# Performance work log

Hardware: AMD Instinct MI355X
Metric: run time of the kernel (lower is better)

Reference implementation:

```python
import jax, jax.numpy as jnp
import numpy as np

B_SZ, SEQ = 2, 4096
D_MODEL = 1024
EXPAND = 2
HEADDIM = 64
D_STATE = 128
D_CONV = 4
INTER = EXPAND * D_MODEL            # 2048
NHEADS = INTER // HEADDIM           # 32
CONV_DIM = INTER + 2 * D_STATE      # n_groups = 1
PROJ_DIM = 2 * INTER + 2 * D_STATE + NHEADS
CHUNK = 256
EPS = 1e-5


def setup_inputs() -> dict:
    key = jax.random.key(0)
    k = jax.random.split(key, 6)
    u = jax.random.normal(k[0], (B_SZ, SEQ, D_MODEL), jnp.float32)
    in_proj_w = jax.random.normal(k[1], (D_MODEL, PROJ_DIM), jnp.float32) * 0.02
    conv_w = jax.random.normal(k[2], (CONV_DIM, D_CONV), jnp.float32) * 0.2
    conv_b = jnp.zeros((CONV_DIM,), jnp.float32)
    # dt init in [1e-3, 1e-1], inverse-softplus so softplus(dt_bias) recovers dt
    dt0 = jnp.exp(jax.random.uniform(k[3], (NHEADS,), jnp.float32, np.log(1e-3), np.log(1e-1)))
    dt_bias = jnp.log(jnp.expm1(dt0))
    A_log = jnp.log(jnp.arange(1, NHEADS + 1, dtype=jnp.float32))
    D_param = jnp.ones((NHEADS,), jnp.float32)
    norm_w = jnp.ones((INTER,), jnp.float32)
    out_proj_w = jax.random.normal(k[4], (INTER, D_MODEL), jnp.float32) * 0.02
    return {"u": u, "in_proj_w": in_proj_w, "conv_w": conv_w, "conv_b": conv_b,
            "dt_bias": dt_bias, "A_log": A_log, "D_param": D_param,
            "norm_w": norm_w, "out_proj_w": out_proj_w}


def _silu(x):
    return x * jax.nn.sigmoid(x)


def _causal_conv1d(x, w, b):
    # depthwise causal conv; x (b,s,c), w (c,k); tap k-1 is the current timestep
    k = w.shape[1]
    xp = jnp.pad(x, ((0, 0), (k - 1, 0), (0, 0)))
    y = b
    for i in range(k):
        y = y + xp[:, i:i + x.shape[1], :] * w[:, i]
    return y


def _segsum(x):
    # x (..., l) -> (..., l, l); segsum[i, j] = sum_{j < k <= i} x[k], -inf above diag
    l = x.shape[-1]
    cs = jnp.cumsum(x, -1)
    d = cs[..., :, None] - cs[..., None, :]
    mask = jnp.tril(jnp.ones((l, l), dtype=bool))
    return jnp.where(mask, d, -jnp.inf)


def _ssd(x, dt, A, Bm, Cm):
    # Mamba-2 chunked SSD (ssd_minimal_discrete with X = x*dt, Adt = A*dt).
    # x (b,s,h,p), dt (b,s,h), A (h,), Bm/Cm (b,s,n)
    b, s, h, p = x.shape
    n = Bm.shape[-1]
    c = s // CHUNK
    X = (x * dt[..., None]).reshape(b, c, CHUNK, h, p)          # (b,c,l,h,p)
    Adt = (dt * A).reshape(b, c, CHUNK, h).transpose(0, 3, 1, 2)  # (b,h,c,l)
    Bc = Bm.reshape(b, c, CHUNK, n)
    Cc = Cm.reshape(b, c, CHUNK, n)
    A_cum = jnp.cumsum(Adt, -1)                                  # (b,h,c,l)
    L = jnp.exp(_segsum(Adt))                                    # (b,h,c,l,l) causal decay
    # intra-chunk (diagonal blocks)
    scores = jnp.einsum('bcln,bcsn->bcls', Cc, Bc)               # (b,c,l,l)
    Y_diag = jnp.einsum('bhcls,bcshp->bclhp', scores[:, None] * L, X)
    # per-chunk final states
    decay_states = jnp.exp(A_cum[..., -1:] - A_cum)              # (b,h,c,l)
    states = jnp.einsum('bcln,bhcl,bclhp->bchpn', Bc, decay_states, X)
    # inter-chunk recurrence on chunk states
    A_chunk = jnp.pad(A_cum[..., -1], ((0, 0), (0, 0), (1, 0)))  # (b,h,c+1)
    decay_chunk = jnp.exp(_segsum(A_chunk))                      # (b,h,c+1,c+1)
    states = jnp.concatenate([jnp.zeros_like(states[:, :1]), states], axis=1)  # (b,c+1,h,p,n)
    states = jnp.einsum('bhzc,bchpn->bzhpn', decay_chunk, states)[:, :-1]      # (b,c,h,p,n)
    # state -> output contribution
    Y_off = jnp.einsum('bcln,bchpn,bhcl->bclhp', Cc, states, jnp.exp(A_cum))
    return (Y_diag + Y_off).reshape(b, s, h, p)


def reference(u, in_proj_w, conv_w, conv_b, dt_bias, A_log, D_param, norm_w, out_proj_w):
    b, s, _ = u.shape
    zxbcdt = u @ in_proj_w                                       # (b,s,PROJ_DIM)
    z = zxbcdt[..., :INTER]
    xBC = zxbcdt[..., INTER:INTER + CONV_DIM]
    dt = zxbcdt[..., INTER + CONV_DIM:]
    xBC = _silu(_causal_conv1d(xBC, conv_w, conv_b))
    x = xBC[..., :INTER]
    Bm = xBC[..., INTER:INTER + D_STATE]
    Cm = xBC[..., INTER + D_STATE:]
    dt = jax.nn.softplus(dt + dt_bias)                           # (b,s,h)
    A = -jnp.exp(A_log)                                          # (h,)
    xh = x.reshape(b, s, NHEADS, HEADDIM)
    y = _ssd(xh, dt, A, Bm, Cm) + D_param[None, None, :, None] * xh
    y = y.reshape(b, s, INTER)
    g = y * _silu(z)                                             # gated RMSNorm
    g = g * jax.lax.rsqrt(jnp.mean(g * g, -1, keepdims=True) + EPS) * norm_w
    return g @ out_proj_w
```

## Files before the change

kernel.cpp:

```cpp
#include <hip/hip_runtime.h>
#include <hip/hip_bf16.h>

#define B_SZ 2
#define SEQ 4096
#define DMODEL 1024
#define INTER 2048
#define NHEADS 32
#define HDIM 64
#define DSTATE 128
#define DCONV 4
#define CONVDIM 2304
#define PROJDIM 4384
#define CHUNK 256
#define NCHUNK 16
#define ROWS (B_SZ*SEQ)
#define NGEMM 4352

typedef __hip_bfloat16 bf16;
typedef short bfx8 __attribute__((ext_vector_type(8)));
typedef float f32x4 __attribute__((ext_vector_type(4)));

__device__ __forceinline__ float sigmoidf_(float x){ return 1.f/(1.f+expf(-x)); }
__device__ __forceinline__ float b2f(bf16 v){ return __bfloat162float(v); }
__device__ __forceinline__ bf16 f2b(float v){ return __float2bfloat16(v); }
__device__ __forceinline__ float bits2f(unsigned short u){ return __uint_as_float(((unsigned)u) << 16); }
__device__ __forceinline__ unsigned short f2bits(float v){ bf16 t = __float2bfloat16(v); return *(unsigned short*)&t; }

#define MFMA16(a,b,c) __builtin_amdgcn_mfma_f32_16x16x32_bf16(a,b,c,0,0,0)

__global__ void zero_out_kernel(float* o, int n){
  int i = blockIdx.x*256 + threadIdx.x;
  if (i < n) o[i] = 0.f;
}

__global__ __launch_bounds__(256) void castu_kernel(const float* __restrict__ in,
    unsigned short* __restrict__ o){
  int i = blockIdx.x*256 + threadIdx.x;
  float4 v = ((const float4*)in)[i];
  ushort4 w;
  w.x = f2bits(v.x); w.y = f2bits(v.y); w.z = f2bits(v.z); w.w = f2bits(v.w);
  ((ushort4*)o)[i] = w;
}

__global__ __launch_bounds__(256) void transcast_kernel(const float* __restrict__ in,
    bf16* __restrict__ outT, int R, int ld, int coff){
  __shared__ float t[64][65];
  int r0 = blockIdx.y*64, c0 = blockIdx.x*64;
  int tid = threadIdx.x;
  #pragma unroll
  for (int i = 0; i < 16; i++){
    int idx = tid + i*256;
    int r = idx >> 6, c = idx & 63;
    t[r][c] = in[(size_t)(r0+r)*ld + coff + c0 + c];
  }
  __syncthreads();
  #pragma unroll
  for (int i = 0; i < 16; i++){
    int idx = tid + i*256;
    int c = idx >> 6, r = idx & 63;
    outT[(size_t)(c0+c)*R + r0 + r] = f2b(t[r][c]);
  }
}

__device__ __forceinline__ void stage8(const bf16* __restrict__ g, int Kdim,
    int tile0, int k0, char* region, int h, int tid){
  #pragma unroll
  for (int l = 0; l < 2; l++){
    int o  = h*16384 + (l*512 + tid)*16;
    int os = o ^ (((o >> 7) & 7) << 4);
    const bf16* src = g + (size_t)(tile0 + (os >> 7))*Kdim + k0 + ((os & 127) >> 1);
    __builtin_amdgcn_global_load_lds(
      (const __attribute__((address_space(1))) void*)src,
      (__attribute__((address_space(3))) void*)(region + h*16384 + (l*512 + (tid >> 6)*64)*16),
      16, 0, 0);
  }
}
__device__ __forceinline__ bfx8 fr8(const char* region, int row, int colbyte){
  int o = row*128 + colbyte;
  o ^= ((row & 7) << 4);
  return *(const bfx8*)(region + o);
}

#define LGKM0  asm volatile("s_waitcnt lgkmcnt(0)" ::: "memory"); __builtin_amdgcn_sched_barrier(0)
#define VM4    asm volatile("s_waitcnt vmcnt(4)" ::: "memory")
#define BAR    __builtin_amdgcn_s_barrier()
#define PRIO1  __builtin_amdgcn_s_setprio(1)
#define PRIO0  __builtin_amdgcn_s_setprio(0)

#define MFMA_QUAD(MH, NH, BARR)                                                \
  PRIO1;                                                                       \
  _Pragma("unroll") for (int m = 0; m < 4; m++)                                \
    _Pragma("unroll") for (int n = 0; n < 2; n++)                              \
      _Pragma("unroll") for (int kk = 0; kk < 2; kk++)                         \
        acc[(MH)+m][(NH)+n] = MFMA16(aF[m][kk], BARR[n][kk], acc[(MH)+m][(NH)+n]); \
  PRIO0

#define GEMM8_BODY(K_, NBX_, EPILOGUE)                                         \
  extern __shared__ char lds[];                                                \
  char* A0 = lds;          char* B0 = lds + 32768;                             \
  char* A1 = lds + 65536;  char* B1 = lds + 98304;                             \
  const int tid = threadIdx.x, lane = tid & 63, wid = tid >> 6;                \
  const int wm = wid >> 2, wn = wid & 3;                                       \
  int nb = (blockIdx.x & 7)*((int)gridDim.x >> 3) + (blockIdx.x >> 3);         \
  const int bx = nb % (NBX_), by = nb / (NBX_);                                \
  const int row0 = by*256, col0 = bx*256;                                      \
  f32x4 acc[8][4] = {};                                                        \
  bfx8 aF[4][2], b01[2][2], b23[2][2];                                         \
  const int frow = lane & 15;                                                  \
  const int fcb0 = (lane >> 4)*16;                                             \
  stage8(Bt, K_, col0, 0,  B0, 0, tid);                                        \
  stage8(Bt, K_, col0, 0,  B0, 1, tid);                                        \
  stage8(A,  K_, row0, 0,  A0, 0, tid);                                        \
  stage8(A,  K_, row0, 0,  A0, 1, tid);                                        \
  stage8(Bt, K_, col0, 64, B1, 0, tid);                                        \
  stage8(Bt, K_, col0, 64, B1, 1, tid);                                        \
  VM4;                                                                         \
  BAR;                                                                         \
  _Pragma("unroll 1")                                                          \
  for (int j = 0; j < (K_)/128; j++){                                          \
    const int kO  = j*128 + 64;                                                \
    const int kS1 = (j*128 + 128) & ((K_) - 1);                                \
    const int kS2 = (j*128 + 192) & ((K_) - 1);                                \
    stage8(A, K_, row0, kO, A1, 0, tid);                                       \
    _Pragma("unroll") for (int m = 0; m < 4; m++)                              \
      _Pragma("unroll") for (int kk = 0; kk < 2; kk++)                         \
        aF[m][kk] = fr8(A0, wm*128 + m*16 + frow, kk*64 + fcb0);               \
    _Pragma("unroll") for (int n = 0; n < 2; n++)                              \
      _Pragma("unroll") for (int kk = 0; kk < 2; kk++)                         \
        b01[n][kk] = fr8(B0, wn*64 + n*16 + frow, kk*64 + fcb0);               \
    LGKM0;                                                                     \
    MFMA_QUAD(0, 0, b01);                                                      \
    BAR;                                                                       \
    stage8(A, K_, row0, kO, A1, 1, tid);                                       \
    _Pragma("unroll") for (int n = 0; n < 2; n++)                              \
      _Pragma("unroll") for (int kk = 0; kk < 2; kk++)                         \
        b23[n][kk] = fr8(B0, wn*64 + (n+2)*16 + frow, kk*64 + fcb0);           \
    LGKM0;                                                                     \
    MFMA_QUAD(0, 2, b23);                                                      \
    BAR;                                                                       \
    stage8(Bt, K_, col0, kS1, B0, 0, tid);                                     \
    _Pragma("unroll") for (int m = 0; m < 4; m++)                              \
      _Pragma("unroll") for (int kk = 0; kk < 2; kk++)                         \
        aF[m][kk] = fr8(A0, wm*128 + (m+4)*16 + frow, kk*64 + fcb0);           \
    LGKM0;                                                                     \
    MFMA_QUAD(4, 0, b01);                                                      \
    BAR;                                                                       \
    stage8(Bt, K_, col0, kS1, B0, 1, tid);                                     \
    VM4;                                                                       \
    MFMA_QUAD(4, 2, b23);                                                      \
    BAR;                                                                       \
    stage8(A, K_, row0, kS1, A0, 0, tid);                                      \
    _Pragma("unroll") for (int m = 0; m < 4; m++)                              \
      _Pragma("unroll") for (int kk = 0; kk < 2; kk++)                         \
        aF[m][kk] = fr8(A1, wm*128 + m*16 + frow, kk*64 + fcb0);               \
    _Pragma("unroll") for (int n = 0; n < 2; n++)                              \
      _Pragma("unroll") for (int kk = 0; kk < 2; kk++)                         \
        b01[n][kk] = fr8(B1, wn*64 + n*16 + frow, kk*64 + fcb0);               \
    LGKM0;                                                                     \
    MFMA_QUAD(0, 0, b01);                                                      \
    BAR;                                                                       \
    stage8(A, K_, row0, kS1, A0, 1, tid);                                      \
    _Pragma("unroll") for (int n = 0; n < 2; n++)                              \
      _Pragma("unroll") for (int kk = 0; kk < 2; kk++)                         \
        b23[n][kk] = fr8(B1, wn*64 + (n+2)*16 + frow, kk*64 + fcb0);           \
    LGKM0;                                                                     \
    MFMA_QUAD(0, 2, b23);                                                      \
    BAR;                                                                       \
    stage8(Bt, K_, col0, kS2, B1, 0, tid);                                     \
    _Pragma("unroll") for (int m = 0; m < 4; m++)                              \
      _Pragma("unroll") for (int kk = 0; kk < 2; kk++)                         \
        aF[m][kk] = fr8(A1, wm*128 + (m+4)*16 + frow, kk*64 + fcb0);           \
    LGKM0;                                                                     \
    MFMA_QUAD(4, 0, b01);                                                      \
    BAR;                                                                       \
    stage8(Bt, K_, col0, kS2, B1, 1, tid);                                     \
    VM4;                                                                       \
    MFMA_QUAD(4, 2, b23);                                                      \
    BAR;                                                                       \
  }                                                                            \
  _Pragma("unroll") for (int m = 0; m < 8; m++){                               \
    int row = row0 + wm*128 + m*16 + (lane >> 4)*4;                            \
    _Pragma("unroll") for (int n = 0; n < 4; n++){                             \
      int col = col0 + wn*64 + n*16 + (lane & 15);                             \
      _Pragma("unroll") for (int r = 0; r < 4; r++){                           \
        float v = acc[m][n][r];                                                \
        int rr = row + r;                                                      \
        EPILOGUE                                                               \
      }                                                                        \
    }                                                                          \
  }

__global__ __launch_bounds__(512, 2) void gemm8_inproj(const bf16* __restrict__ A,
    const bf16* __restrict__ Bt, bf16* __restrict__ z, bf16* __restrict__ xbc){
  GEMM8_BODY(DMODEL, 17,
    if (col < INTER) z[(size_t)rr*INTER + col] = f2b(v);
    else             xbc[(size_t)rr*CONVDIM + (col - INTER)] = f2b(v);
  )
}
__global__ __launch_bounds__(512, 2) void gemm8_outproj(const bf16* __restrict__ A,
    const bf16* __restrict__ Bt, float* __restrict__ C){
  GEMM8_BODY(INTER, 4,
    C[(size_t)rr*DMODEL + col] = v;
  )
}

#define MFMA_GEMM_BODY(K_, EPILOGUE)                                           \
  __shared__ unsigned short As[128*64];                                        \
  __shared__ unsigned short Bs[128*64];                                        \
  const int tid = threadIdx.x;                                                 \
  const int lane = tid & 63, wid = tid >> 6;                                   \
  const int wm = wid >> 1, wn = wid & 1;                                       \
  const int row0 = blockIdx.y*128, col0 = blockIdx.x*128;                      \
  f32x4 acc[4][4] = {};                                                        \
  const int rstg = wid*32 + ((lane>>3)&7);                                     \
  const int kstg = (lane&7)*8;                                                 \
  for (int k0 = 0; k0 < (K_); k0 += 64){                                       \
    _Pragma("unroll")                                                          \
    for (int j = 0; j < 4; j++){                                               \
      const bf16* gA = A + (size_t)(row0 + rstg + j*8)*(K_) + k0 + kstg;       \
      __builtin_amdgcn_global_load_lds(                                        \
        (const __attribute__((address_space(1))) void*)gA,                     \
        (__attribute__((address_space(3))) void*)(As + (wid*32 + j*8)*64),     \
        16, 0, 0);                                                             \
      const bf16* gB = Bt + (size_t)(col0 + rstg + j*8)*(K_) + k0 + kstg;      \
      __builtin_amdgcn_global_load_lds(                                        \
        (const __attribute__((address_space(1))) void*)gB,                     \
        (__attribute__((address_space(3))) void*)(Bs + (wid*32 + j*8)*64),     \
        16, 0, 0);                                                             \
    }                                                                          \
    __syncthreads();                                                           \
    _Pragma("unroll")                                                          \
    for (int kk = 0; kk < 2; kk++){                                            \
      bfx8 af[4], bfr[4];                                                      \
      _Pragma("unroll")                                                        \
      for (int m = 0; m < 4; m++)                                              \
        af[m] = *(const bfx8*)(As + (wm*64 + m*16 + (lane&15))*64              \
                               + kk*32 + (lane>>4)*8);                         \
      _Pragma("unroll")                                                        \
      for (int n = 0; n < 4; n++)                                              \
        bfr[n] = *(const bfx8*)(Bs + (wn*64 + n*16 + (lane&15))*64             \
                                + kk*32 + (lane>>4)*8);                        \
      _Pragma("unroll")                                                        \
      for (int m = 0; m < 4; m++)                                              \
        _Pragma("unroll")                                                      \
        for (int n = 0; n < 4; n++)                                            \
          acc[m][n] = MFMA16(af[m], bfr[n], acc[m][n]);                        \
    }                                                                          \
    __syncthreads();                                                           \
  }                                                                            \
  _Pragma("unroll")                                                            \
  for (int m = 0; m < 4; m++){                                                 \
    int row = row0 + wm*64 + m*16 + (lane>>4)*4;                               \
    _Pragma("unroll")                                                          \
    for (int n = 0; n < 4; n++){                                               \
      int col = col0 + wn*64 + n*16 + (lane&15);                               \
      _Pragma("unroll")                                                        \
      for (int r = 0; r < 4; r++){                                             \
        float v = acc[m][n][r];                                                \
        int rr = row + r;                                                      \
        EPILOGUE                                                               \
      }                                                                        \
    }                                                                          \
  }

__global__ __launch_bounds__(256) void gemm_mfma_inproj(const bf16* __restrict__ A,
    const bf16* __restrict__ Bt, bf16* __restrict__ z, bf16* __restrict__ xbc){
  MFMA_GEMM_BODY(DMODEL,
    if (col < INTER) z[(size_t)rr*INTER + col] = f2b(v);
    else             xbc[(size_t)rr*CONVDIM + (col - INTER)] = f2b(v);
  )
}
__global__ __launch_bounds__(256) void gemm_mfma_outproj(const bf16* __restrict__ A,
    const bf16* __restrict__ Bt, float* __restrict__ C){
  MFMA_GEMM_BODY(INTER,
    C[(size_t)rr*DMODEL + col] = v;
  )
}

__global__ __launch_bounds__(256) void dt_partial(const float* __restrict__ u,
    const float* __restrict__ w_in, float* __restrict__ partial){
  __shared__ float wsm[128][33];
  __shared__ float us[64][133];
  int ks = blockIdx.x, row0 = blockIdx.y*64;
  int k0 = ks*128;
  int tid = threadIdx.x;
  #pragma unroll
  for (int i = 0; i < 16; i++){
    int idx = tid + i*256;
    int r = idx >> 5, c = idx & 31;
    wsm[r][c] = w_in[(size_t)(k0 + r)*PROJDIM + NGEMM + c];
  }
  #pragma unroll
  for (int i = 0; i < 8; i++){
    int idx = tid + i*256;
    int r = idx >> 5, c4 = idx & 31;
    float4 v = *(const float4*)(u + (size_t)(row0 + r)*DMODEL + k0 + c4*4);
    us[r][c4*4+0] = v.x; us[r][c4*4+1] = v.y; us[r][c4*4+2] = v.z; us[r][c4*4+3] = v.w;
  }
  __syncthreads();
  int col = tid & 31, r0 = tid >> 5;
  float acc[8] = {};
  #pragma unroll 4
  for (int kk4 = 0; kk4 < 32; kk4++){
    float4 uv[8];
    #pragma unroll
    for (int i = 0; i < 8; i++)
      uv[i] = *(const float4*)&us[r0 + i*8][kk4*4];
    #pragma unroll
    for (int j = 0; j < 4; j++){
      float wv = wsm[kk4*4 + j][col];
      #pragma unroll
      for (int i = 0; i < 8; i++){
        float uvj = (j == 0) ? uv[i].x : (j == 1) ? uv[i].y : (j == 2) ? uv[i].z : uv[i].w;
        acc[i] = fmaf(uvj, wv, acc[i]);
      }
    }
  }
  #pragma unroll
  for (int i = 0; i < 8; i++)
    partial[((size_t)ks*ROWS + row0 + r0 + i*8)*NHEADS + col] = acc[i];
}

__global__ __launch_bounds__(256) void dt_reduce(const float* __restrict__ partial,
    float* __restrict__ dtraw){
  int idx = blockIdx.x*256 + threadIdx.x;
  float s = 0.f;
  #pragma unroll
  for (int ks = 0; ks < 8; ks++)
    s += partial[(size_t)ks*ROWS*NHEADS + idx];
  dtraw[idx] = s;
}

__global__ __launch_bounds__(256) void conv_kernel(const bf16* __restrict__ xbc,
    const float* __restrict__ cw, const float* __restrict__ cb,
    bf16* __restrict__ x, bf16* __restrict__ Bm, bf16* __restrict__ Cm){
  int bt = blockIdx.x / 9;
  int ch = (blockIdx.x % 9)*256 + threadIdx.x;
  int t = bt & (SEQ-1);
  float acc = cb[ch];
  #pragma unroll
  for (int i = 0; i < 4; i++){
    int tt = t - 3 + i;
    if (tt >= 0)
      acc = fmaf(b2f(xbc[(size_t)(bt - t + tt)*CONVDIM + ch]), cw[ch*4+i], acc);
  }
  float v = acc * sigmoidf_(acc);
  if (ch < INTER)              x[(size_t)bt*INTER + ch] = f2b(v);
  else if (ch < INTER+DSTATE)  Bm[(size_t)bt*DSTATE + (ch-INTER)] = f2b(v);
  else                         Cm[(size_t)bt*DSTATE + (ch-INTER-DSTATE)] = f2b(v);
}

__global__ __launch_bounds__(256) void dt_kernel(const float* __restrict__ dtraw,
    const float* __restrict__ dt_bias, float* __restrict__ dt){
  int idx = blockIdx.x*256 + threadIdx.x;
  int h = idx & 31;
  float v = dtraw[idx] + dt_bias[h];
  dt[idx] = (v > 20.f) ? v : log1pf(expf(v));
}

__global__ __launch_bounds__(256) void acum_kernel(const float* __restrict__ dt,
    const float* __restrict__ A_log, float* __restrict__ Acum){
  int bi = blockIdx.x;
  int c = bi & 15; int h = (bi >> 4) & 31; int b = bi >> 9;
  int l = threadIdx.x;
  __shared__ float sbuf[CHUNK];
  float A = -expf(A_log[h]);
  int t = c*CHUNK + l;
  sbuf[l] = dt[(size_t)(b*SEQ + t)*NHEADS + h] * A;
  __syncthreads();
  for (int off = 1; off < CHUNK; off <<= 1){
    float add = (l >= off) ? sbuf[l-off] : 0.f;
    __syncthreads();
    sbuf[l] += add;
    __syncthreads();
  }
  Acum[(size_t)bi*CHUNK + l] = sbuf[l];
}

__global__ __launch_bounds__(256) void scores_mfma(const bf16* __restrict__ Bm,
    const bf16* __restrict__ Cm, bf16* __restrict__ S){
  int bc = blockIdx.x;
  int rb = blockIdx.y;
  int b = bc >> 4, c = bc & 15;
  int tid = threadIdx.x, lane = tid & 63, k = tid >> 6;
  if (k > rb) return;
  const bf16* Crow = Cm + (size_t)(b*SEQ + c*CHUNK)*DSTATE;
  const bf16* Brow = Bm + (size_t)(b*SEQ + c*CHUNK)*DSTATE;
  f32x4 acc[4][4] = {};
  #pragma unroll
  for (int kk = 0; kk < 4; kk++){
    bfx8 af[4], bfr[4];
    #pragma unroll
    for (int m = 0; m < 4; m++)
      af[m] = *(const bfx8*)(Crow + (size_t)(rb*64 + m*16 + (lane&15))*DSTATE + kk*32 + (lane>>4)*8);
    #pragma unroll
    for (int n = 0; n < 4; n++)
      bfr[n] = *(const bfx8*)(Brow + (size_t)(k*64 + n*16 + (lane&15))*DSTATE + kk*32 + (lane>>4)*8);
    #pragma unroll
    for (int m = 0; m < 4; m++)
      #pragma unroll
      for (int n = 0; n < 4; n++)
        acc[m][n] = MFMA16(af[m], bfr[n], acc[m][n]);
  }
  bf16* dst = S + (size_t)bc*CHUNK*CHUNK;
  #pragma unroll
  for (int m = 0; m < 4; m++)
    #pragma unroll
    for (int n = 0; n < 4; n++)
      #pragma unroll
      for (int r = 0; r < 4; r++)
        dst[(size_t)(rb*64 + m*16 + (lane>>4)*4 + r)*CHUNK + k*64 + n*16 + (lane&15)]
          = f2b(acc[m][n][r]);
}

__global__ __launch_bounds__(256) void xwt_kernel(const bf16* __restrict__ x,
    const bf16* __restrict__ Bm, const float* __restrict__ dt,
    const float* __restrict__ Acum, bf16* __restrict__ xwt, bf16* __restrict__ bt){
  int pt = blockIdx.x, tt = blockIdx.y, b = blockIdx.z;
  int tid = threadIdx.x;
  __shared__ unsigned short tile[64][72];
  __shared__ float wf[64];
  int t0 = tt*64;
  if (pt < 32){
    int h = pt, c = t0 >> 8;
    if (tid < 64){
      const float* AcB = Acum + ((size_t)(b*NHEADS + h)*NCHUNK + c)*CHUNK;
      int t = t0 + tid;
      wf[tid] = dt[(size_t)(b*SEQ + t)*NHEADS + h] * expf(AcB[255] - AcB[t & 255]);
    }
    __syncthreads();
    const bf16* src = x + (size_t)(b*SEQ + t0)*INTER + pt*64;
    #pragma unroll
    for (int i = 0; i < 2; i++){
      int u = tid + i*256;
      int r = u >> 3, po = (u & 7)*8;
      bfx8 v = *(const bfx8*)(src + (size_t)r*INTER + po);
      float d = wf[r];
      #pragma unroll
      for (int j = 0; j < 8; j++)
        tile[r][po + j] = f2bits(bits2f((unsigned short)v[j]) * d);
    }
    __syncthreads();
    bf16* dst = xwt + ((size_t)(b*INTER) + pt*64)*SEQ + t0;
    #pragma unroll
    for (int i = 0; i < 2; i++){
      int u = tid + i*256;
      int p = u >> 3, tc = (u & 7)*8;
      bfx8 v;
      #pragma unroll
      for (int j = 0; j < 8; j++) v[j] = (short)tile[tc + j][p];
      *(bfx8*)(dst + (size_t)p*SEQ + tc) = v;
    }
  } else {
    int n0 = (pt - 32)*64;
    const bf16* src = Bm + (size_t)(b*SEQ + t0)*DSTATE + n0;
    #pragma unroll
    for (int i = 0; i < 2; i++){
      int u = tid + i*256;
      int r = u >> 3, po = (u & 7)*8;
      bfx8 v = *(const bfx8*)(src + (size_t)r*DSTATE + po);
      *(bfx8*)&tile[r][po] = v;
    }
    __syncthreads();
    bf16* dst = bt + ((size_t)(b*DSTATE) + n0)*SEQ + t0;
    #pragma unroll
    for (int i = 0; i < 2; i++){
      int u = tid + i*256;
      int p = u >> 3, tc = (u & 7)*8;
      bfx8 v;
      #pragma unroll
      for (int j = 0; j < 8; j++) v[j] = (short)tile[tc + j][p];
      *(bfx8*)(dst + (size_t)p*SEQ + tc) = v;
    }
  }
}

__global__ __launch_bounds__(256) void chunk_states_mfma(const bf16* __restrict__ xwt,
    const bf16* __restrict__ bt, float* __restrict__ states){
  int bi = blockIdx.x;
  int h = bi & 31; int c = (bi >> 5) & 15; int b = bi >> 9;
  int tid = threadIdx.x, lane = tid & 63, w = tid >> 6;
  int wm = w >> 1, wn = w & 1;
  const bf16* Arow = xwt + ((size_t)(b*INTER) + h*64)*SEQ + c*CHUNK;
  const bf16* Brow = bt + (size_t)(b*DSTATE)*SEQ + c*CHUNK;
  f32x4 acc[2][4] = {};
  #pragma unroll
  for (int kk = 0; kk < 8; kk++){
    bfx8 af[2], bfr[4];
    #pragma unroll
    for (int m = 0; m < 2; m++)
      af[m] = *(const bfx8*)(Arow + (size_t)(wm*32 + m*16 + (lane&15))*SEQ + kk*32 + (lane>>4)*8);
    #pragma unroll
    for (int n = 0; n < 4; n++)
      bfr[n] = *(const bfx8*)(Brow + (size_t)(wn*64 + n*16 + (lane&15))*SEQ + kk*32 + (lane>>4)*8);
    #pragma unroll
    for (int m = 0; m < 2; m++)
      #pragma unroll
      for (int n = 0; n < 4; n++)
        acc[m][n] = MFMA16(af[m], bfr[n], acc[m][n]);
  }
  float* dst = states + (size_t)bi*HDIM*DSTATE;
  #pragma unroll
  for (int m = 0; m < 2; m++)
    #pragma unroll
    for (int n = 0; n < 4; n++)
      #pragma unroll
      for (int r = 0; r < 4; r++){
        int p = wm*32 + m*16 + (lane>>4)*4 + r;
        int nn = wn*64 + n*16 + (lane&15);
        dst[(size_t)p*DSTATE + nn] = acc[m][n][r];
      }
}

__global__ __launch_bounds__(256) void scan_kernel(float* __restrict__ states,
    const float* __restrict__ Acum){
  int idx = blockIdx.x*256 + threadIdx.x;
  int n = idx & 127; int p = (idx >> 7) & 63; int h = (idx >> 13) & 31; int b = idx >> 18;
  float R = 0.f;
  for (int c = 0; c < NCHUNK; c++){
    size_t o = (((size_t)((b*NCHUNK + c)*NHEADS + h))*HDIM + p)*DSTATE + n;
    float s = states[o];
    states[o] = R;
    float dA = expf(Acum[((size_t)(b*NHEADS + h)*NCHUNK + c)*CHUNK + CHUNK-1]);
    R = R*dA + s;
  }
}

__global__ __launch_bounds__(256, 3) void ydiag_mfma(
    const bf16* x, const float* __restrict__ dt,
    const float* __restrict__ Acum, const bf16* __restrict__ Sg,
    const bf16* __restrict__ Cm, const float* __restrict__ states,
    const float* __restrict__ Dp, bf16* y){
  int bi = blockIdx.x;
  int h = bi & 31; int c = (bi >> 5) & 15; int b = bi >> 9;
  int bc = b*NCHUNK + c;
  int tid = threadIdx.x, lane = tid & 63, w = tid >> 6;

  __shared__ unsigned short XdtT[64*264];
  __shared__ unsigned short pool[128*72];
  __shared__ float Acs[CHUNK];
  __shared__ float dts[CHUNK];

  const float* AcBase = Acum + ((size_t)(b*NHEADS + h)*NCHUNK + c)*CHUNK;
  Acs[tid] = AcBase[tid];
  dts[tid] = dt[(size_t)(b*SEQ + c*CHUNK + tid)*NHEADS + h];
  {
    const float* src = states + (size_t)bi*HDIM*DSTATE;
    #pragma unroll
    for (int i = 0; i < 32; i++){
      int idx = tid + i*256;
      int p = idx >> 7, n = idx & 127;
      pool[p*136 + n] = f2bits(src[idx]);
    }
  }
  __syncthreads();

  const bf16* Crow = Cm + (size_t)(b*SEQ + c*CHUNK)*DSTATE;

  f32x4 accY[4][4] = {};
  #pragma unroll
  for (int kk = 0; kk < 4; kk++){
    bfx8 af[4], bfr[4];
    #pragma unroll
    for (int m = 0; m < 4; m++)
      af[m] = *(const bfx8*)(Crow + (size_t)(w*64 + m*16 + (lane&15))*DSTATE + kk*32 + (lane>>4)*8);
    #pragma unroll
    for (int n = 0; n < 4; n++)
      bfr[n] = *(const bfx8*)(pool + (n*16 + (lane&15))*136 + kk*32 + (lane>>4)*8);
    #pragma unroll
    for (int m = 0; m < 4; m++)
      #pragma unroll
      for (int n = 0; n < 4; n++)
        accY[m][n] = MFMA16(af[m], bfr[n], accY[m][n]);
  }
  {
    float eAl[4][4];
    #pragma unroll
    for (int m = 0; m < 4; m++)
      #pragma unroll
      for (int r = 0; r < 4; r++)
        eAl[m][r] = expf(Acs[w*64 + m*16 + (lane>>4)*4 + r]);
    #pragma unroll
    for (int m = 0; m < 4; m++)
      #pragma unroll
      for (int n = 0; n < 4; n++)
        #pragma unroll
        for (int r = 0; r < 4; r++)
          accY[m][n][r] *= eAl[m][r];
  }
  __syncthreads();

  #pragma unroll 1
  for (int q = 0; q < 2; q++){
    const bf16* xg = x + (size_t)(b*SEQ + c*CHUNK + q*128)*INTER + h*HDIM;
    #pragma unroll
    for (int i = 0; i < 4; i++){
      int u = tid + i*256;
      int s = u >> 3, p0 = (u & 7)*8;
      bfx8 v = *(const bfx8*)(xg + (size_t)s*INTER + p0);
      float d = dts[q*128 + s];
      bfx8 o;
      #pragma unroll
      for (int j = 0; j < 8; j++)
        o[j] = (short)f2bits(bits2f((unsigned short)v[j]) * d);
      *(bfx8*)(pool + s*72 + p0) = o;
    }
    __syncthreads();
    {
      int p = tid & 63, sb = tid >> 6;
      #pragma unroll
      for (int i = 0; i < 4; i++){
        int s0 = (sb + i*4)*8;
        bfx8 v;
        #pragma unroll
        for (int j = 0; j < 8; j++)
          v[j] = (short)pool[(s0 + j)*72 + p];
        *(bfx8*)(XdtT + p*264 + q*128 + s0) = v;
      }
    }
    __syncthreads();
  }

  const bf16* Srow = Sg + (size_t)bc*CHUNK*CHUNK + (size_t)(w*64)*CHUNK;
  float Dh = Dp[h];
  for (int j = 0; j <= w; j++){
    int s0 = j*64;
    bfx8 wfr[4][2];
    if (j < w){
      float m_ = Acs[s0 + 63];
      float rowf[4];
      #pragma unroll
      for (int m = 0; m < 4; m++)
        rowf[m] = expf(Acs[w*64 + m*16 + (lane&15)] - m_);
      #pragma unroll
      for (int kk = 0; kk < 2; kk++){
        float colf[8];
        #pragma unroll
        for (int t = 0; t < 8; t++)
          colf[t] = expf(m_ - Acs[s0 + kk*32 + (lane>>4)*8 + t]);
        #pragma unroll
        for (int m = 0; m < 4; m++){
          bfx8 raw = *(const bfx8*)(Srow + (size_t)(m*16 + (lane&15))*CHUNK + s0 + kk*32 + (lane>>4)*8);
          bfx8 o;
          #pragma unroll
          for (int t = 0; t < 8; t++)
            o[t] = (short)f2bits(bits2f((unsigned short)raw[t]) * rowf[m] * colf[t]);
          wfr[m][kk] = o;
        }
      }
    } else {
      #pragma unroll
      for (int kk = 0; kk < 2; kk++)
        #pragma unroll
        for (int m = 0; m < 4; m++){
          int lg = w*64 + m*16 + (lane&15);
          float Al = Acs[lg];
          bfx8 raw = *(const bfx8*)(Srow + (size_t)(m*16 + (lane&15))*CHUNK + s0 + kk*32 + (lane>>4)*8);
          bfx8 o;
          #pragma unroll
          for (int t = 0; t < 8; t++){
            int sg = s0 + kk*32 + (lane>>4)*8 + t;
            float v;
            if (sg > lg)       v = 0.f;
            else if (sg == lg) v = bits2f((unsigned short)raw[t]) + Dh/dts[lg];
            else               v = bits2f((unsigned short)raw[t]) * expf(Al - Acs[sg]);
            o[t] = (short)f2bits(v);
          }
          wfr[m][kk] = o;
        }
    }
    #pragma unroll
    for (int kk = 0; kk < 2; kk++){
      bfx8 bfr[4];
      #pragma unroll
      for (int n = 0; n < 4; n++)
        bfr[n] = *(const bfx8*)(XdtT + (n*16 + (lane&15))*264 + s0 + kk*32 + (lane>>4)*8);
      #pragma unroll
      for (int m = 0; m < 4; m++)
        #pragma unroll
        for (int n = 0; n < 4; n++)
          accY[m][n] = MFMA16(wfr[m][kk], bfr[n], accY[m][n]);
    }
  }
  bf16* yg = y + (size_t)(b*SEQ + c*CHUNK)*INTER + h*HDIM;
  #pragma unroll
  for (int m = 0; m < 4; m++)
    #pragma unroll
    for (int n = 0; n < 4; n++)
      #pragma unroll
      for (int r = 0; r < 4; r++)
        yg[(size_t)(w*64 + m*16 + (lane>>4)*4 + r)*INTER + n*16 + (lane&15)]
          = f2b(accY[m][n][r]);
}

__global__ __launch_bounds__(256) void gatenorm_kernel(bf16* __restrict__ y,
    const bf16* __restrict__ z, const float* __restrict__ nw){
  int row = blockIdx.x;
  const bf16* zr = z + (size_t)row*INTER;
  bf16* yr = y + (size_t)row*INTER;
  int tid = threadIdx.x;
  float g[8]; float ss = 0.f;
  #pragma unroll
  for (int i = 0; i < 8; i++){
    int idx = tid + i*256;
    float zv = b2f(zr[idx]);
    float gv = b2f(yr[idx]) * zv * sigmoidf_(zv);
    g[i] = gv; ss += gv*gv;
  }
  #pragma unroll
  for (int off = 32; off > 0; off >>= 1) ss += __shfl_down(ss, off);
  __shared__ float red[4];
  __shared__ float stot;
  int lane = tid & 63, wid = tid >> 6;
  if (lane == 0) red[wid] = ss;
  __syncthreads();
  if (tid == 0) stot = rsqrtf((red[0]+red[1]+red[2]+red[3]) * (1.f/INTER) + 1e-5f);
  __syncthreads();
  float sc = stot;
  #pragma unroll
  for (int i = 0; i < 8; i++){
    int idx = tid + i*256;
    yr[idx] = f2b(g[i]*sc*nw[idx]);
  }
}

extern "C" void kernel_launch(void* const* d_in, const int* in_sizes, int n_in,
                              void* d_out, int out_size, void* d_ws, size_t ws_size,
                              hipStream_t stream){
  const float* u    = (const float*)d_in[0];
  const float* w_in = (const float*)d_in[1];
  const float* cw   = (const float*)d_in[2];
  const float* cb   = (const float*)d_in[3];
  const float* dtb  = (const float*)d_in[4];
  const float* Alog = (const float*)d_in[5];
  const float* Dp   = (const float*)d_in[6];
  const float* nw   = (const float*)d_in[7];
  const float* w_out= (const float*)d_in[8];
  float* out = (float*)d_out;
  char* ws = (char*)d_ws;

  const size_t OFF_Z     = 0;
  const size_t OFF_XBC   = 33554432;
  const size_t OFF_DT    = 67108864;
  const size_t OFF_ACUM  = 68157440;
  const size_t OFF_X     = 71303168;
  const size_t OFF_UBF   = 104857600;
  const size_t OFF_WINT  = 121634816;
  const size_t OFF_XWT   = 104857600;
  const size_t OFF_BM    = 138412032;
  const size_t OFF_CM    = 140509184;
  const size_t OFF_DTRAW = 142606336;
  const size_t OFF_BT    = 143654912;
  const size_t OFF_WOUTT = 145752064;
  const size_t OFF_PART  = 149946368;
  const size_t NEED      = 158334976;

  if (ws_size < NEED){
    zero_out_kernel<<<(out_size + 255)/256, 256, 0, stream>>>(out, out_size);
    return;
  }

  bf16*  z      = (bf16*)(ws + OFF_Z);
  bf16*  xbc    = (bf16*)(ws + OFF_XBC);
  float* states = (float*)(ws + OFF_XBC);
  float* dt     = (float*)(ws + OFF_DT);
  float* Acum   = (float*)(ws + OFF_ACUM);
  bf16*  x      = (bf16*)(ws + OFF_X);
  bf16*  y      = (bf16*)(ws + OFF_X);
  bf16*  u_bf   = (bf16*)(ws + OFF_UBF);
  bf16*  w_inT  = (bf16*)(ws + OFF_WINT);
  bf16*  xwt    = (bf16*)(ws + OFF_XWT);
  bf16*  Bm     = (bf16*)(ws + OFF_BM);
  bf16*  Cm     = (bf16*)(ws + OFF_CM);
  float* dtraw  = (float*)(ws + OFF_DTRAW);
  bf16*  bt     = (bf16*)(ws + OFF_BT);
  bf16*  w_outT = (bf16*)(ws + OFF_WOUTT);
  float* part   = (float*)(ws + OFF_PART);
  bf16*  S      = (bf16*)(ws + OFF_PART);

  bool use8 = true;
  if (hipFuncSetAttribute((const void*)gemm8_inproj,
        hipFuncAttributeMaxDynamicSharedMemorySize, 131072) != hipSuccess) use8 = false;
  if (hipFuncSetAttribute((const void*)gemm8_outproj,
        hipFuncAttributeMaxDynamicSharedMemorySize, 131072) != hipSuccess) use8 = false;

  castu_kernel<<<(ROWS*DMODEL/4)/256, 256, 0, stream>>>(u, (unsigned short*)u_bf);
  transcast_kernel<<<dim3(NGEMM/64, DMODEL/64), 256, 0, stream>>>(w_in, w_inT, DMODEL, PROJDIM, 0);
  if (use8)
    gemm8_inproj<<<544, 512, 131072, stream>>>(u_bf, w_inT, z, xbc);
  else
    gemm_mfma_inproj<<<dim3(NGEMM/128, ROWS/128), 256, 0, stream>>>(u_bf, w_inT, z, xbc);
  dt_partial<<<dim3(8, ROWS/64), 256, 0, stream>>>(u, w_in, part);
  dt_reduce<<<(ROWS*NHEADS)/256, 256, 0, stream>>>(part, dtraw);
  conv_kernel<<<ROWS*9, 256, 0, stream>>>(xbc, cw, cb, x, Bm, Cm);
  scores_mfma<<<dim3(B_SZ*NCHUNK, 4), 256, 0, stream>>>(Bm, Cm, S);
  dt_kernel<<<ROWS*NHEADS/256, 256, 0, stream>>>(dtraw, dtb, dt);
  acum_kernel<<<B_SZ*NHEADS*NCHUNK, 256, 0, stream>>>(dt, Alog, Acum);
  xwt_kernel<<<dim3(34, 64, 2), 256, 0, stream>>>(x, Bm, dt, Acum, xwt, bt);
  chunk_states_mfma<<<B_SZ*NCHUNK*NHEADS, 256, 0, stream>>>(xwt, bt, states);
  scan_kernel<<<(B_SZ*NHEADS*HDIM*DSTATE)/256, 256, 0, stream>>>(states, Acum);
  ydiag_mfma<<<B_SZ*NCHUNK*NHEADS, 256, 0, stream>>>(x, dt, Acum, S, Cm, states, Dp, y);
  transcast_kernel<<<dim3(DMODEL/64, INTER/64), 256, 0, stream>>>(w_out, w_outT, INTER, DMODEL, 0);
  gatenorm_kernel<<<ROWS, 256, 0, stream>>>(y, z, nw);
  if (use8)
    gemm8_outproj<<<128, 512, 131072, stream>>>(y, w_outT, out);
  else
    gemm_mfma_outproj<<<dim3(DMODEL/128, ROWS/128), 256, 0, stream>>>(y, w_outT, out);
}
```

Baseline: 425.3 us.

## Fuse small dt kernels, stage GEMM epilogue via LDS, and trim wasted prefetches

Several unrelated changes land together. The bf16 cast of u moves into dt_partial, and dt_reduce, dt_kernel and acum_kernel merge into one acum_fused kernel, which removes launches and intermediate buffers. The in-projection GEMM epilogue now goes through LDS so each thread writes 16-byte coalesced rows instead of scattered 2-byte stores. The GEMM main loop skips the redundant wrap-around prefetches on its last iteration. scores_mfma packs its 10 lower-triangular tiles into 3 blocks so fewer warps exit idle. The costs are extra barriers in the epilogue and more branching in the GEMM loop.

```diff
diff --git a/kernel.cpp b/kernel.cpp
--- a/kernel.cpp
+++ b/kernel.cpp
@@ -33,15 +33,6 @@
   if (i < n) o[i] = 0.f;
 }
 
-__global__ __launch_bounds__(256) void castu_kernel(const float* __restrict__ in,
-    unsigned short* __restrict__ o){
-  int i = blockIdx.x*256 + threadIdx.x;
-  float4 v = ((const float4*)in)[i];
-  ushort4 w;
-  w.x = f2bits(v.x); w.y = f2bits(v.y); w.z = f2bits(v.z); w.w = f2bits(v.w);
-  ((ushort4*)o)[i] = w;
-}
-
 __global__ __launch_bounds__(256) void transcast_kernel(const float* __restrict__ in,
     bf16* __restrict__ outT, int R, int ld, int coff){
   __shared__ float t[64][65];
@@ -83,6 +74,7 @@
 
 #define LGKM0  asm volatile("s_waitcnt lgkmcnt(0)" ::: "memory"); __builtin_amdgcn_sched_barrier(0)
 #define VM4    asm volatile("s_waitcnt vmcnt(4)" ::: "memory")
+#define VM0    asm volatile("s_waitcnt vmcnt(0)" ::: "memory")
 #define BAR    __builtin_amdgcn_s_barrier()
 #define PRIO1  __builtin_amdgcn_s_setprio(1)
 #define PRIO0  __builtin_amdgcn_s_setprio(0)
@@ -95,7 +87,7 @@
         acc[(MH)+m][(NH)+n] = MFMA16(aF[m][kk], BARR[n][kk], acc[(MH)+m][(NH)+n]); \
   PRIO0
 
-#define GEMM8_BODY(K_, NBX_, EPILOGUE)                                         \
+#define GEMM8_BODY(K_, NBX_)                                                   \
   extern __shared__ char lds[];                                                \
   char* A0 = lds;          char* B0 = lds + 32768;                             \
   char* A1 = lds + 65536;  char* B1 = lds + 98304;                             \
@@ -108,6 +100,7 @@
   bfx8 aF[4][2], b01[2][2], b23[2][2];                                         \
   const int frow = lane & 15;                                                  \
   const int fcb0 = (lane >> 4)*16;                                             \
+  const int JLAST = (K_)/128 - 1;                                              \
   stage8(Bt, K_, col0, 0,  B0, 0, tid);                                        \
   stage8(Bt, K_, col0, 0,  B0, 1, tid);                                        \
   stage8(A,  K_, row0, 0,  A0, 0, tid);                                        \
@@ -117,7 +110,7 @@
   VM4;                                                                         \
   BAR;                                                                         \
   _Pragma("unroll 1")                                                          \
-  for (int j = 0; j < (K_)/128; j++){                                          \
+  for (int j = 0; j <= JLAST; j++){                                            \
     const int kO  = j*128 + 64;                                                \
     const int kS1 = (j*128 + 128) & ((K_) - 1);                                \
     const int kS2 = (j*128 + 192) & ((K_) - 1);                                \
@@ -138,18 +131,18 @@
     LGKM0;                                                                     \
     MFMA_QUAD(0, 2, b23);                                                      \
     BAR;                                                                       \
-    stage8(Bt, K_, col0, kS1, B0, 0, tid);                                     \
+    if (j < JLAST) stage8(Bt, K_, col0, kS1, B0, 0, tid);                      \
     _Pragma("unroll") for (int m = 0; m < 4; m++)                              \
       _Pragma("unroll") for (int kk = 0; kk < 2; kk++)                         \
         aF[m][kk] = fr8(A0, wm*128 + (m+4)*16 + frow, kk*64 + fcb0);           \
     LGKM0;                                                                     \
     MFMA_QUAD(4, 0, b01);                                                      \
     BAR;                                                                       \
-    stage8(Bt, K_, col0, kS1, B0, 1, tid);                                     \
-    VM4;                                                                       \
+    if (j < JLAST){ stage8(Bt, K_, col0, kS1, B0, 1, tid); VM4; }              \
+    else { VM0; }                                                              \
     MFMA_QUAD(4, 2, b23);                                                      \
     BAR;                                                                       \
-    stage8(A, K_, row0, kS1, A0, 0, tid);                                      \
+    if (j < JLAST) stage8(A, K_, row0, kS1, A0, 0, tid);                       \
     _Pragma("unroll") for (int m = 0; m < 4; m++)                              \
       _Pragma("unroll") for (int kk = 0; kk < 2; kk++)                         \
         aF[m][kk] = fr8(A1, wm*128 + m*16 + frow, kk*64 + fcb0);               \
@@ -159,49 +152,72 @@
     LGKM0;                                                                     \
     MFMA_QUAD(0, 0, b01);                                                      \
     BAR;                                                                       \
-    stage8(A, K_, row0, kS1, A0, 1, tid);                                      \
+    if (j < JLAST) stage8(A, K_, row0, kS1, A0, 1, tid);                       \
     _Pragma("unroll") for (int n = 0; n < 2; n++)                              \
       _Pragma("unroll") for (int kk = 0; kk < 2; kk++)                         \
         b23[n][kk] = fr8(B1, wn*64 + (n+2)*16 + frow, kk*64 + fcb0);           \
     LGKM0;                                                                     \
     MFMA_QUAD(0, 2, b23);                                                      \
     BAR;                                                                       \
-    stage8(Bt, K_, col0, kS2, B1, 0, tid);                                     \
+    if (j < JLAST) stage8(Bt, K_, col0, kS2, B1, 0, tid);                      \
     _Pragma("unroll") for (int m = 0; m < 4; m++)                              \
       _Pragma("unroll") for (int kk = 0; kk < 2; kk++)                         \
         aF[m][kk] = fr8(A1, wm*128 + (m+4)*16 + frow, kk*64 + fcb0);           \
     LGKM0;                                                                     \
     MFMA_QUAD(4, 0, b01);                                                      \
     BAR;                                                                       \
-    stage8(Bt, K_, col0, kS2, B1, 1, tid);                                     \
+    if (j < JLAST) stage8(Bt, K_, col0, kS2, B1, 1, tid);                      \
     VM4;                                                                       \
     MFMA_QUAD(4, 2, b23);                                                      \
     BAR;                                                                       \
-  }                                                                            \
-  _Pragma("unroll") for (int m = 0; m < 8; m++){                               \
-    int row = row0 + wm*128 + m*16 + (lane >> 4)*4;                            \
-    _Pragma("unroll") for (int n = 0; n < 4; n++){                             \
-      int col = col0 + wn*64 + n*16 + (lane & 15);                             \
-      _Pragma("unroll") for (int r = 0; r < 4; r++){                           \
-        float v = acc[m][n][r];                                                \
-        int rr = row + r;                                                      \
-        EPILOGUE                                                               \
-      }                                                                        \
-    }                                                                          \
-  }
+  }
+
+#define SST_STRIDE 280
 
 __global__ __launch_bounds__(512, 2) void gemm8_inproj(const bf16* __restrict__ A,
     const bf16* __restrict__ Bt, bf16* __restrict__ z, bf16* __restrict__ xbc){
-  GEMM8_BODY(DMODEL, 17,
-    if (col < INTER) z[(size_t)rr*INTER + col] = f2b(v);
-    else             xbc[(size_t)rr*CONVDIM + (col - INTER)] = f2b(v);
-  )
+  GEMM8_BODY(DMODEL, 17)
+  unsigned short* sst = (unsigned short*)lds;
+  #pragma unroll 1
+  for (int half = 0; half < 2; half++){
+    if (wm == half){
+      #pragma unroll
+      for (int m = 0; m < 8; m++)
+        #pragma unroll
+        for (int n = 0; n < 4; n++)
+          #pragma unroll
+          for (int r = 0; r < 4; r++){
+            int rl = m*16 + (lane>>4)*4 + r;
+            sst[rl*SST_STRIDE + wn*64 + n*16 + (lane&15)] = f2bits(acc[m][n][r]);
+          }
+    }
+    BAR;
+    #pragma unroll
+    for (int i = 0; i < 8; i++){
+      int q = tid + i*512;
+      int rl = q >> 5, c8 = (q & 31)*8;
+      bfx8 v = *(const bfx8*)(sst + rl*SST_STRIDE + c8);
+      int gr = row0 + half*128 + rl, gc = col0 + c8;
+      if (gc < INTER) *(bfx8*)(z + (size_t)gr*INTER + gc) = v;
+      else            *(bfx8*)(xbc + (size_t)gr*CONVDIM + (gc - INTER)) = v;
+    }
+    BAR;
+  }
 }
 __global__ __launch_bounds__(512, 2) void gemm8_outproj(const bf16* __restrict__ A,
     const bf16* __restrict__ Bt, float* __restrict__ C){
-  GEMM8_BODY(INTER, 4,
-    C[(size_t)rr*DMODEL + col] = v;
-  )
+  GEMM8_BODY(INTER, 4)
+  #pragma unroll
+  for (int m = 0; m < 8; m++){
+    int row = row0 + wm*128 + m*16 + (lane >> 4)*4;
+    #pragma unroll
+    for (int n = 0; n < 4; n++){
+      int col = col0 + wn*64 + n*16 + (lane & 15);
+      #pragma unroll
+      for (int r = 0; r < 4; r++)
+        C[(size_t)(row + r)*DMODEL + col] = acc[m][n][r];
+    }
+  }
 }
 
 #define MFMA_GEMM_BODY(K_, EPILOGUE)                                           \
@@ -278,7 +294,8 @@
 }
 
 __global__ __launch_bounds__(256) void dt_partial(const float* __restrict__ u,
-    const float* __restrict__ w_in, float* __restrict__ partial){
+    const float* __restrict__ w_in, float* __restrict__ partial,
+    unsigned short* __restrict__ u_bf){
   __shared__ float wsm[128][33];
   __shared__ float us[64][133];
   int ks = blockIdx.x, row0 = blockIdx.y*64;
@@ -296,6 +313,9 @@
     int r = idx >> 5, c4 = idx & 31;
     float4 v = *(const float4*)(u + (size_t)(row0 + r)*DMODEL + k0 + c4*4);
     us[r][c4*4+0] = v.x; us[r][c4*4+1] = v.y; us[r][c4*4+2] = v.z; us[r][c4*4+3] = v.w;
+    ushort4 w;
+    w.x = f2bits(v.x); w.y = f2bits(v.y); w.z = f2bits(v.z); w.w = f2bits(v.w);
+    *(ushort4*)(u_bf + (size_t)(row0 + r)*DMODEL + k0 + c4*4) = w;
   }
   __syncthreads();
   int col = tid & 31, r0 = tid >> 5;
@@ -319,16 +339,6 @@
   #pragma unroll
   for (int i = 0; i < 8; i++)
     partial[((size_t)ks*ROWS + row0 + r0 + i*8)*NHEADS + col] = acc[i];
-}
-
-__global__ __launch_bounds__(256) void dt_reduce(const float* __restrict__ partial,
-    float* __restrict__ dtraw){
-  int idx = blockIdx.x*256 + threadIdx.x;
-  float s = 0.f;
-  #pragma unroll
-  for (int ks = 0; ks < 8; ks++)
-    s += partial[(size_t)ks*ROWS*NHEADS + idx];
-  dtraw[idx] = s;
 }
 
 __global__ __launch_bounds__(256) void conv_kernel(const bf16* __restrict__ xbc,
@@ -350,23 +360,23 @@
   else                         Cm[(size_t)bt*DSTATE + (ch-INTER-DSTATE)] = f2b(v);
 }
 
-__global__ __launch_bounds__(256) void dt_kernel(const float* __restrict__ dtraw,
-    const float* __restrict__ dt_bias, float* __restrict__ dt){
-  int idx = blockIdx.x*256 + threadIdx.x;
-  int h = idx & 31;
-  float v = dtraw[idx] + dt_bias[h];
-  dt[idx] = (v > 20.f) ? v : log1pf(expf(v));
-}
-
-__global__ __launch_bounds__(256) void acum_kernel(const float* __restrict__ dt,
-    const float* __restrict__ A_log, float* __restrict__ Acum){
+__global__ __launch_bounds__(256) void acum_fused(const float* __restrict__ partial,
+    const float* __restrict__ dt_bias, const float* __restrict__ A_log,
+    float* __restrict__ dt, float* __restrict__ Acum){
   int bi = blockIdx.x;
   int c = bi & 15; int h = (bi >> 4) & 31; int b = bi >> 9;
   int l = threadIdx.x;
   __shared__ float sbuf[CHUNK];
+  int t = c*CHUNK + l;
+  size_t idx = (size_t)(b*SEQ + t)*NHEADS + h;
+  float s = dt_bias[h];
+  #pragma unroll
+  for (int ks = 0; ks < 8; ks++)
+    s += partial[(size_t)ks*ROWS*NHEADS + idx];
+  float v = (s > 20.f) ? s : log1pf(expf(s));
+  dt[idx] = v;
   float A = -expf(A_log[h]);
-  int t = c*CHUNK + l;
-  sbuf[l] = dt[(size_t)(b*SEQ + t)*NHEADS + h] * A;
+  sbuf[l] = v * A;
   __syncthreads();
   for (int off = 1; off < CHUNK; off <<= 1){
     float add = (l >= off) ? sbuf[l-off] : 0.f;
@@ -380,10 +390,12 @@
 __global__ __launch_bounds__(256) void scores_mfma(const bf16* __restrict__ Bm,
     const bf16* __restrict__ Cm, bf16* __restrict__ S){
   int bc = blockIdx.x;
-  int rb = blockIdx.y;
   int b = bc >> 4, c = bc & 15;
-  int tid = threadIdx.x, lane = tid & 63, k = tid >> 6;
-  if (k > rb) return;
+  int tid = threadIdx.x, lane = tid & 63;
+  int task = blockIdx.y*4 + (tid >> 6);
+  if (task >= 10) return;
+  int rb = (task >= 6) ? 3 : (task >= 3) ? 2 : (task >= 1) ? 1 : 0;
+  int j = task - rb*(rb+1)/2;
   const bf16* Crow = Cm + (size_t)(b*SEQ + c*CHUNK)*DSTATE;
   const bf16* Brow = Bm + (size_t)(b*SEQ + c*CHUNK)*DSTATE;
   f32x4 acc[4][4] = {};
@@ -395,7 +407,7 @@
       af[m] = *(const bfx8*)(Crow + (size_t)(rb*64 + m*16 + (lane&15))*DSTATE + kk*32 + (lane>>4)*8);
     #pragma unroll
     for (int n = 0; n < 4; n++)
-      bfr[n] = *(const bfx8*)(Brow + (size_t)(k*64 + n*16 + (lane&15))*DSTATE + kk*32 + (lane>>4)*8);
+      bfr[n] = *(const bfx8*)(Brow + (size_t)(j*64 + n*16 + (lane&15))*DSTATE + kk*32 + (lane>>4)*8);
     #pragma unroll
     for (int m = 0; m < 4; m++)
       #pragma unroll
@@ -409,7 +421,7 @@
     for (int n = 0; n < 4; n++)
       #pragma unroll
       for (int r = 0; r < 4; r++)
-        dst[(size_t)(rb*64 + m*16 + (lane>>4)*4 + r)*CHUNK + k*64 + n*16 + (lane&15)]
+        dst[(size_t)(rb*64 + m*16 + (lane>>4)*4 + r)*CHUNK + j*64 + n*16 + (lane&15)]
           = f2b(acc[m][n][r]);
 }
 
@@ -749,7 +761,6 @@
   const size_t OFF_XWT   = 104857600;
   const size_t OFF_BM    = 138412032;
   const size_t OFF_CM    = 140509184;
-  const size_t OFF_DTRAW = 142606336;
   const size_t OFF_BT    = 143654912;
   const size_t OFF_WOUTT = 145752064;
   const size_t OFF_PART  = 149946368;
@@ -772,7 +783,6 @@
   bf16*  xwt    = (bf16*)(ws + OFF_XWT);
   bf16*  Bm     = (bf16*)(ws + OFF_BM);
   bf16*  Cm     = (bf16*)(ws + OFF_CM);
-  float* dtraw  = (float*)(ws + OFF_DTRAW);
   bf16*  bt     = (bf16*)(ws + OFF_BT);
   bf16*  w_outT = (bf16*)(ws + OFF_WOUTT);
   float* part   = (float*)(ws + OFF_PART);
@@ -784,18 +794,15 @@
   if (hipFuncSetAttribute((const void*)gemm8_outproj,
         hipFuncAttributeMaxDynamicSharedMemorySize, 131072) != hipSuccess) use8 = false;
 
-  castu_kernel<<<(ROWS*DMODEL/4)/256, 256, 0, stream>>>(u, (unsigned short*)u_bf);
+  dt_partial<<<dim3(8, ROWS/64), 256, 0, stream>>>(u, w_in, part, (unsigned short*)u_bf);
   transcast_kernel<<<dim3(NGEMM/64, DMODEL/64), 256, 0, stream>>>(w_in, w_inT, DMODEL, PROJDIM, 0);
   if (use8)
     gemm8_inproj<<<544, 512, 131072, stream>>>(u_bf, w_inT, z, xbc);
   else
     gemm_mfma_inproj<<<dim3(NGEMM/128, ROWS/128), 256, 0, stream>>>(u_bf, w_inT, z, xbc);
-  dt_partial<<<dim3(8, ROWS/64), 256, 0, stream>>>(u, w_in, part);
-  dt_reduce<<<(ROWS*NHEADS)/256, 256, 0, stream>>>(part, dtraw);
   conv_kernel<<<ROWS*9, 256, 0, stream>>>(xbc, cw, cb, x, Bm, Cm);
-  scores_mfma<<<dim3(B_SZ*NCHUNK, 4), 256, 0, stream>>>(Bm, Cm, S);
-  dt_kernel<<<ROWS*NHEADS/256, 256, 0, stream>>>(dtraw, dtb, dt);
-  acum_kernel<<<B_SZ*NHEADS*NCHUNK, 256, 0, stream>>>(dt, Alog, Acum);
+  acum_fused<<<B_SZ*NHEADS*NCHUNK, 256, 0, stream>>>(part, dtb, Alog, dt, Acum);
+  scores_mfma<<<dim3(B_SZ*NCHUNK, 3), 256, 0, stream>>>(Bm, Cm, S);
   xwt_kernel<<<dim3(34, 64, 2), 256, 0, stream>>>(x, Bm, dt, Acum, xwt, bt);
   chunk_states_mfma<<<B_SZ*NCHUNK*NHEADS, 256, 0, stream>>>(xwt, bt, states);
   scan_kernel<<<(B_SZ*NHEADS*HDIM*DSTATE)/256, 256, 0, stream>>>(states, Acum);
```

After: 419.5 us. About the same (-1.4%).
